# Kernel tuning notes

Measured on AMD Instinct MI355X. Metric: run time of the kernel, lower is better.

Reference implementation:

```python
import jax, jax.numpy as jnp
import numpy as np

HEADS = 16
LN_EPS = 1e-5


def setup_inputs() -> dict:
    key = jax.random.key(0)
    ks = jax.random.split(key, 12)
    B, IMG, Q, H = 8192, 2048, 768, 1024
    def init(k, shape, fan_in):
        return jax.random.normal(k, shape, dtype=jnp.float32) * (fan_in ** -0.5)
    return {
        "features1": jax.random.normal(ks[0], (B, IMG), dtype=jnp.float32),
        "features2": jax.random.normal(ks[1], (B, Q), dtype=jnp.float32),
        "W1": init(ks[2], (IMG, H), IMG),
        "b1": jnp.zeros((H,), dtype=jnp.float32),
        "W2": init(ks[3], (Q, H), Q),
        "b2": jnp.zeros((H,), dtype=jnp.float32),
        "Wqkv": init(ks[4], (H, 3 * H), H),
        "Wout": init(ks[5], (H, H), H),
        "bout": jnp.zeros((H,), dtype=jnp.float32),
        "gamma": jnp.ones((2 * H,), dtype=jnp.float32),
        "beta": jnp.zeros((2 * H,), dtype=jnp.float32),
    }


def reference(features1, features2, W1, b1, W2, b2, Wqkv, Wout, bout, gamma, beta):
    B = features1.shape[0]
    H = W1.shape[1]
    hd = H // HEADS
    scale = hd ** -0.5
    # modality projections -> [B, H] each
    f1 = features1 @ W1 + b1
    f2 = features2 @ W2 + b2
    x = jnp.stack([f1, f2], axis=1)                      # [B, 2, H]
    qkv = x @ Wqkv                                       # [B, 2, 3H]
    q, k, v = jnp.split(qkv, 3, axis=-1)
    # b n (h d) -> b h n d
    def to_heads(t):
        return t.reshape(B, 2, HEADS, hd).transpose(0, 2, 1, 3)
    q, k, v = to_heads(q) * scale, to_heads(k), to_heads(v)
    attn = jnp.einsum('bhid,bhjd->bhij', q, k)           # [B, h, 2, 2]
    attn = jax.nn.softmax(attn, axis=-1)
    out = jnp.einsum('bhij,bhjd->bhid', attn, v)         # [B, h, 2, d]
    out = out.transpose(0, 2, 1, 3).reshape(B, 2, H)     # b h n d -> b n (h d)
    out = out @ Wout + bout                              # [B, 2, H]
    flat = out.reshape(B, 2 * H)
    # LayerNorm over last dim
    mu = jnp.mean(flat, axis=-1, keepdims=True)
    var = jnp.var(flat, axis=-1, keepdims=True)
    normed = (flat - mu) * jax.lax.rsqrt(var + LN_EPS) * gamma + beta
    # dropout in eval mode = identity
    res = jnp.concatenate([f1, f2], axis=1)              # [B, 2H]
    return normed + res
```

## Files before the change

kernel.cpp:

```cpp
#include <hip/hip_runtime.h>
#include <hip/hip_bf16.h>
#include <cstdint>

typedef __attribute__((ext_vector_type(8))) short short8;
typedef __attribute__((ext_vector_type(4))) short short4v;
typedef __attribute__((ext_vector_type(4))) float floatx4;
typedef __attribute__((ext_vector_type(4))) unsigned short ushort4v;

__device__ __forceinline__ float bf2f(unsigned short u) {
    union { unsigned int u; float f; } v;
    v.u = ((unsigned int)u) << 16;
    return v.f;
}
__device__ __forceinline__ unsigned short f2bf(float f) {
    union { float f; unsigned int u; } v; v.f = f;
    unsigned int u = v.u;
    unsigned int r = (u + 0x7FFFu + ((u >> 16) & 1u)) >> 16;
    return (unsigned short)r;
}
__device__ __forceinline__ float lo_bf(unsigned int u) {
    union { unsigned int u; float f; } v; v.u = u << 16; return v.f;
}
__device__ __forceinline__ float hi_bf(unsigned int u) {
    union { unsigned int u; float f; } v; v.u = u & 0xffff0000u; return v.f;
}
__device__ __forceinline__ void gld_lds16(const void* g, void* l) {
    __builtin_amdgcn_global_load_lds(
        (const __attribute__((address_space(1))) unsigned int*)g,
        (__attribute__((address_space(3))) unsigned int*)l,
        16, 0, 0);
}

__global__ __launch_bounds__(256) void cvt_bf16_kernel(const float* __restrict__ in,
                                                       unsigned short* __restrict__ out,
                                                       int n4) {
    int i = blockIdx.x * 256 + threadIdx.x;
    if (i >= n4) return;
    float4 v = ((const float4*)in)[i];
    ushort4v o;
    o.x = f2bf(v.x); o.y = f2bf(v.y); o.z = f2bf(v.z); o.w = f2bf(v.w);
    ((ushort4v*)out)[i] = o;
}

__global__ __launch_bounds__(256) void transpose_cvt_kernel(const float* __restrict__ in,
                                                            unsigned short* __restrict__ out,
                                                            int K, int N) {
    __shared__ float tile[32][33];
    const int n0 = blockIdx.x * 32;
    const int k0 = blockIdx.y * 32;
    const int tx = threadIdx.x;
    const int ty = threadIdx.y;
#pragma unroll
    for (int i = 0; i < 32; i += 8)
        tile[ty + i][tx] = in[(size_t)(k0 + ty + i) * N + n0 + tx];
    __syncthreads();
#pragma unroll
    for (int i = 0; i < 32; i += 8)
        out[(size_t)(n0 + ty + i) * K + k0 + tx] = f2bf(tile[tx][ty + i]);
}

template <bool OUT_BF16, bool HAS_BIAS>
__global__ __launch_bounds__(256, 2)
void gemm_bt64(const unsigned short* __restrict__ A, const unsigned short* __restrict__ Bt,
               void* __restrict__ Cv, const float* __restrict__ bias,
               int M, int N, int K, int ldc) {
    __shared__ alignas(16) unsigned short As[8192];
    __shared__ alignas(16) unsigned short Bs[8192];

    const int tid  = threadIdx.x;
    const int lane = tid & 63;
    const int wave = tid >> 6;
    const int blockM = blockIdx.y * 128;
    const int blockN = blockIdx.x * 128;
    const int wm = wave >> 1, wn = wave & 1;

    const unsigned short* gA[4];
    const unsigned short* gB[4];
    unsigned short* lA[4];
    unsigned short* lB[4];
#pragma unroll
    for (int g = 0; g < 4; g++) {
        int ci = g * 256 + tid;
        int hh = ci >> 9, rem = ci & 511, row = rem >> 2, sub = rem & 3;
        gA[g] = A  + (size_t)(blockM + row) * K + hh * 32 + sub * 8;
        gB[g] = Bt + (size_t)(blockN + row) * K + hh * 32 + sub * 8;
        lA[g] = As + g * 2048 + wave * 512;
        lB[g] = Bs + g * 2048 + wave * 512;
    }

    floatx4 acc[4][4];
#pragma unroll
    for (int i = 0; i < 4; i++)
#pragma unroll
        for (int j = 0; j < 4; j++) acc[i][j] = (floatx4){0.f, 0.f, 0.f, 0.f};

    const int col  = lane & 15;
    const int quad = lane >> 4;
    const int aoff32 = (wm * 64 + col) * 32 + quad * 8;
    const int boff32 = (wn * 64 + col) * 32 + quad * 8;

    const int kIters = K >> 6;
    for (int kt = 0; kt < kIters; ++kt) {
        const size_t ko = (size_t)kt * 64;
#pragma unroll
        for (int g = 0; g < 4; g++) gld_lds16(gA[g] + ko, lA[g]);
#pragma unroll
        for (int g = 0; g < 4; g++) gld_lds16(gB[g] + ko, lB[g]);
        __syncthreads();

#pragma unroll
        for (int hh = 0; hh < 2; hh++) {
            short8 a[4], b[4];
#pragma unroll
            for (int i = 0; i < 4; i++) a[i] = *(const short8*)&As[hh * 4096 + aoff32 + i * 512];
#pragma unroll
            for (int j = 0; j < 4; j++) b[j] = *(const short8*)&Bs[hh * 4096 + boff32 + j * 512];
#pragma unroll
            for (int i = 0; i < 4; i++)
#pragma unroll
                for (int j = 0; j < 4; j++)
                    acc[i][j] = __builtin_amdgcn_mfma_f32_16x16x32_bf16(a[i], b[j], acc[i][j], 0, 0, 0);
        }
        __syncthreads();
    }

#pragma unroll
    for (int i = 0; i < 4; i++) {
#pragma unroll
        for (int j = 0; j < 4; j++) {
#pragma unroll
            for (int r = 0; r < 4; r++) {
                int row = blockM + wm * 64 + i * 16 + quad * 4 + r;
                int cn  = blockN + wn * 64 + j * 16 + col;
                float v = acc[i][j][r];
                if (HAS_BIAS) v += bias[cn];
                if (OUT_BF16) ((unsigned short*)Cv)[(size_t)row * ldc + cn] = f2bf(v);
                else          ((float*)Cv)[(size_t)row * ldc + cn] = v;
            }
        }
    }
}

#define T2_STRIDE 132
__global__ __launch_bounds__(256, 2)
void gemm_qkv_attn(const unsigned short* __restrict__ A, const unsigned short* __restrict__ Bt,
                   unsigned short* __restrict__ attn_out) {
    __shared__ alignas(16) char smem[52224];
    unsigned short* As = (unsigned short*)smem;
    unsigned short* Bs = As + 8192;
    unsigned short* T2 = (unsigned short*)smem;
    float* wsm = (float*)(smem + 50688);

    const int tid  = threadIdx.x;
    const int lane = tid & 63;
    const int wave = tid >> 6;
    const int h = blockIdx.x;
    const int blockM = blockIdx.y * 128;
    const int wm = wave >> 1, wn = wave & 1;
    const int K = 1024;

    const unsigned short* gA[4];
    unsigned short* lA[4];
#pragma unroll
    for (int g = 0; g < 4; g++) {
        int ci = g * 256 + tid;
        int hh = ci >> 9, rem = ci & 511, row = rem >> 2, sub = rem & 3;
        gA[g] = A + (size_t)(blockM + row) * K + hh * 32 + sub * 8;
        lA[g] = As + g * 2048 + wave * 512;
    }
    const unsigned short* gB[6];
    unsigned short* lB[6];
#pragma unroll
    for (int g = 0; g < 6; g++) {
        int ci = g * 256 + tid;
        int hh = (ci >= 768) ? 1 : 0;
        int rem = ci - hh * 768;
        int row = rem >> 2, sub = rem & 3;
        int sec = row >> 6, wr = row & 63;
        gB[g] = Bt + (size_t)(sec * 1024 + h * 64 + wr) * K + hh * 32 + sub * 8;
        lB[g] = Bs + g * 2048 + wave * 512;
    }

    floatx4 acc[4][6];
#pragma unroll
    for (int i = 0; i < 4; i++)
#pragma unroll
        for (int j = 0; j < 6; j++) acc[i][j] = (floatx4){0.f, 0.f, 0.f, 0.f};

    const int col  = lane & 15;
    const int quad = lane >> 4;
    const int aoff32 = (wm * 64 + col) * 32 + quad * 8;
    const int boff32 = (wn * 96 + col) * 32 + quad * 8;

    for (int kt = 0; kt < 16; ++kt) {
        const size_t ko = (size_t)kt * 64;
#pragma unroll
        for (int g = 0; g < 4; g++) gld_lds16(gA[g] + ko, lA[g]);
#pragma unroll
        for (int g = 0; g < 6; g++) gld_lds16(gB[g] + ko, lB[g]);
        __syncthreads();

#pragma unroll
        for (int hh = 0; hh < 2; hh++) {
            short8 a[4], b[6];
#pragma unroll
            for (int i = 0; i < 4; i++) a[i] = *(const short8*)&As[hh * 4096 + aoff32 + i * 512];
#pragma unroll
            for (int j = 0; j < 6; j++) b[j] = *(const short8*)&Bs[hh * 6144 + boff32 + j * 512];
#pragma unroll
            for (int i = 0; i < 4; i++)
#pragma unroll
                for (int j = 0; j < 6; j++)
                    acc[i][j] = __builtin_amdgcn_mfma_f32_16x16x32_bf16(a[i], b[j], acc[i][j], 0, 0, 0);
        }
        __syncthreads();
    }

#pragma unroll
    for (int i = 0; i < 4; i++) {
#pragma unroll
        for (int j = 0; j < 6; j++) {
            int c  = wn * 96 + j * 16 + col;
            int r0 = wm * 64 + i * 16 + quad * 4;
            short4v pk;
            pk.x = (short)f2bf(acc[i][j][0]);
            pk.y = (short)f2bf(acc[i][j][1]);
            pk.z = (short)f2bf(acc[i][j][2]);
            pk.w = (short)f2bf(acc[i][j][3]);
            *(short4v*)&T2[c * T2_STRIDE + r0] = pk;
        }
    }
    __syncthreads();

    if (tid < 64) {
        const int ib = tid;
        float s00 = 0.f, s01 = 0.f, s10 = 0.f, s11 = 0.f;
#pragma unroll 8
        for (int d = 0; d < 64; d++) {
            unsigned int qp = *(const unsigned int*)&T2[d * T2_STRIDE + 2 * ib];
            unsigned int kp = *(const unsigned int*)&T2[(64 + d) * T2_STRIDE + 2 * ib];
            float q0 = lo_bf(qp), q1 = hi_bf(qp);
            float k0 = lo_bf(kp), k1 = hi_bf(kp);
            s00 += q0 * k0; s01 += q0 * k1;
            s10 += q1 * k0; s11 += q1 * k1;
        }
        const float sc = 0.125f;
        s00 *= sc; s01 *= sc; s10 *= sc; s11 *= sc;
        float m0 = fmaxf(s00, s01), m1 = fmaxf(s10, s11);
        float e00 = __expf(s00 - m0), e01 = __expf(s01 - m0);
        float e10 = __expf(s10 - m1), e11 = __expf(s11 - m1);
        float i0 = 1.f / (e00 + e01), i1 = 1.f / (e10 + e11);
        wsm[ib * 4 + 0] = e00 * i0; wsm[ib * 4 + 1] = e01 * i0;
        wsm[ib * 4 + 2] = e10 * i1; wsm[ib * 4 + 3] = e11 * i1;
    }
    __syncthreads();

#pragma unroll
    for (int g = 0; g < 4; g++) {
        int chunk = g * 256 + tid;
        int r = chunk >> 3;
        int dc = (chunk & 7) * 8;
        int ib = r >> 1, n = r & 1;
        float w0 = wsm[ib * 4 + n * 2 + 0];
        float w1 = wsm[ib * 4 + n * 2 + 1];
        short8 o;
#pragma unroll
        for (int dd = 0; dd < 8; dd++) {
            unsigned int vp = *(const unsigned int*)&T2[(128 + dc + dd) * T2_STRIDE + 2 * ib];
            o[dd] = (short)f2bf(w0 * lo_bf(vp) + w1 * hi_bf(vp));
        }
        *(short8*)&attn_out[(size_t)(blockM + r) * 1024 + h * 64 + dc] = o;
    }
}

__global__ __launch_bounds__(256) void ln_res_kernel(const unsigned short* __restrict__ proj,
                                                     const unsigned short* __restrict__ xres,
                                                     const float* __restrict__ gamma,
                                                     const float* __restrict__ beta,
                                                     float* __restrict__ out) {
    const int b = blockIdx.x;
    const int tid = threadIdx.x;
    const size_t base = (size_t)b * 2048;
    short8 p8 = ((const short8*)(proj + base))[tid];
    float pv[8];
#pragma unroll
    for (int e = 0; e < 8; e++) pv[e] = bf2f((unsigned short)p8[e]);
    float s = 0.f, ss = 0.f;
#pragma unroll
    for (int e = 0; e < 8; e++) { s += pv[e]; ss += pv[e] * pv[e]; }
#pragma unroll
    for (int off = 32; off > 0; off >>= 1) {
        s  += __shfl_xor(s, off);
        ss += __shfl_xor(ss, off);
    }
    __shared__ float red[8];
    const int wave = tid >> 6;
    if ((tid & 63) == 0) { red[wave] = s; red[4 + wave] = ss; }
    __syncthreads();
    s  = red[0] + red[1] + red[2] + red[3];
    ss = red[4] + red[5] + red[6] + red[7];
    const float mean = s * (1.0f / 2048.0f);
    const float var  = ss * (1.0f / 2048.0f) - mean * mean;
    const float rstd = rsqrtf(var + 1e-5f);

    const float4* g4 = (const float4*)gamma;
    const float4* b4 = (const float4*)beta;
    float4 g0 = g4[2 * tid], g1 = g4[2 * tid + 1];
    float4 be0 = b4[2 * tid], be1 = b4[2 * tid + 1];
    short8 r8 = ((const short8*)(xres + base))[tid];
    float4 o0, o1;
    o0.x = (pv[0] - mean) * rstd * g0.x + be0.x + bf2f((unsigned short)r8[0]);
    o0.y = (pv[1] - mean) * rstd * g0.y + be0.y + bf2f((unsigned short)r8[1]);
    o0.z = (pv[2] - mean) * rstd * g0.z + be0.z + bf2f((unsigned short)r8[2]);
    o0.w = (pv[3] - mean) * rstd * g0.w + be0.w + bf2f((unsigned short)r8[3]);
    o1.x = (pv[4] - mean) * rstd * g1.x + be1.x + bf2f((unsigned short)r8[4]);
    o1.y = (pv[5] - mean) * rstd * g1.y + be1.y + bf2f((unsigned short)r8[5]);
    o1.z = (pv[6] - mean) * rstd * g1.z + be1.z + bf2f((unsigned short)r8[6]);
    o1.w = (pv[7] - mean) * rstd * g1.w + be1.w + bf2f((unsigned short)r8[7]);
    float4* op = (float4*)(out + base);
    op[2 * tid] = o0;
    op[2 * tid + 1] = o1;
}

extern "C" void kernel_launch(void* const* d_in, const int* in_sizes, int n_in,
                              void* d_out, int out_size, void* d_ws, size_t ws_size,
                              hipStream_t stream) {
    (void)in_sizes; (void)n_in; (void)out_size; (void)ws_size;
    const float* features1 = (const float*)d_in[0];
    const float* features2 = (const float*)d_in[1];
    const float* W1   = (const float*)d_in[2];
    const float* b1   = (const float*)d_in[3];
    const float* W2   = (const float*)d_in[4];
    const float* b2   = (const float*)d_in[5];
    const float* Wqkv = (const float*)d_in[6];
    const float* Wout = (const float*)d_in[7];
    const float* bout = (const float*)d_in[8];
    const float* gamma = (const float*)d_in[9];
    const float* beta  = (const float*)d_in[10];
    float* out = (float*)d_out;

    char* ws = (char*)d_ws;
    unsigned short* f1b   = (unsigned short*)(ws);
    unsigned short* f2b   = (unsigned short*)(ws + 33554432);
    unsigned short* W1t   = (unsigned short*)(ws + 46137344);
    unsigned short* W2t   = (unsigned short*)(ws + 50331648);
    unsigned short* Wqkvt = (unsigned short*)(ws + 51904512);
    unsigned short* Woutt = (unsigned short*)(ws + 58195968);
    unsigned short* xb    = (unsigned short*)(ws + 60293120);
    unsigned short* attn  = (unsigned short*)(ws + 93847552);
    unsigned short* projb = (unsigned short*)(ws + 127401984);

    cvt_bf16_kernel<<<16384, 256, 0, stream>>>(features1, f1b, 8192 * 2048 / 4);
    cvt_bf16_kernel<<<6144, 256, 0, stream>>>(features2, f2b, 8192 * 768 / 4);

    transpose_cvt_kernel<<<dim3(1024 / 32, 2048 / 32), dim3(32, 8), 0, stream>>>(W1, W1t, 2048, 1024);
    transpose_cvt_kernel<<<dim3(1024 / 32, 768 / 32),  dim3(32, 8), 0, stream>>>(W2, W2t, 768, 1024);
    transpose_cvt_kernel<<<dim3(3072 / 32, 1024 / 32), dim3(32, 8), 0, stream>>>(Wqkv, Wqkvt, 1024, 3072);
    transpose_cvt_kernel<<<dim3(1024 / 32, 1024 / 32), dim3(32, 8), 0, stream>>>(Wout, Woutt, 1024, 1024);

    gemm_bt64<true, true><<<dim3(8, 64), 256, 0, stream>>>(
        f1b, W1t, (void*)xb, b1, 8192, 1024, 2048, 2048);
    gemm_bt64<true, true><<<dim3(8, 64), 256, 0, stream>>>(
        f2b, W2t, (void*)(xb + 1024), b2, 8192, 1024, 768, 2048);
    gemm_qkv_attn<<<dim3(16, 128), 256, 0, stream>>>(xb, Wqkvt, attn);
    gemm_bt64<true, true><<<dim3(8, 128), 256, 0, stream>>>(
        attn, Woutt, (void*)projb, bout, 16384, 1024, 1024, 1024);
    ln_res_kernel<<<8192, 256, 0, stream>>>(projb, xb, gamma, beta, out);
}
```

Baseline: 405.1 us.

## Merge conversion/transpose launches and fuse two projection GEMMs into one grid

Six conversion and transpose kernels are merged into a single prep kernel that dispatches on block index. The two modality projection GEMMs are combined into one launch using blockIdx.z. Global-to-LDS address setup is simplified to one base pointer plus fixed strides, and launch bounds request higher occupancy. The goal is to cut launch overhead and tail gaps between small kernels, at the risk of register pressure from the raised occupancy targets.

Result: no change. 398.6 us (-1.6%).

```diff
diff --git a/kernel.cpp b/kernel.cpp
--- a/kernel.cpp
+++ b/kernel.cpp
@@ -31,42 +31,56 @@
         16, 0, 0);
 }
 
-__global__ __launch_bounds__(256) void cvt_bf16_kernel(const float* __restrict__ in,
-                                                       unsigned short* __restrict__ out,
-                                                       int n4) {
-    int i = blockIdx.x * 256 + threadIdx.x;
-    if (i >= n4) return;
-    float4 v = ((const float4*)in)[i];
-    ushort4v o;
-    o.x = f2bf(v.x); o.y = f2bf(v.y); o.z = f2bf(v.z); o.w = f2bf(v.w);
-    ((ushort4v*)out)[i] = o;
-}
-
-__global__ __launch_bounds__(256) void transpose_cvt_kernel(const float* __restrict__ in,
-                                                            unsigned short* __restrict__ out,
-                                                            int K, int N) {
+__global__ __launch_bounds__(256) void prep_kernel(
+    const float* __restrict__ f1, const float* __restrict__ f2,
+    unsigned short* __restrict__ f1b, unsigned short* __restrict__ f2b,
+    const float* __restrict__ W1, unsigned short* __restrict__ W1t,
+    const float* __restrict__ W2, unsigned short* __restrict__ W2t,
+    const float* __restrict__ Wqkv, unsigned short* __restrict__ Wqkvt,
+    const float* __restrict__ Wout, unsigned short* __restrict__ Woutt) {
     __shared__ float tile[32][33];
-    const int n0 = blockIdx.x * 32;
-    const int k0 = blockIdx.y * 32;
-    const int tx = threadIdx.x;
-    const int ty = threadIdx.y;
+    const int b = blockIdx.x;
+    const int tid = threadIdx.x;
+
+    if (b < 5632) {
+        const float* in = (b < 4096) ? f1 : f2;
+        unsigned short* outp = (b < 4096) ? f1b : f2b;
+        int base = ((b < 4096) ? b : (b - 4096)) * 1024 + tid;
+#pragma unroll
+        for (int it = 0; it < 4; it++) {
+            int i = base + it * 256;
+            float4 v = ((const float4*)in)[i];
+            ushort4v o;
+            o.x = f2bf(v.x); o.y = f2bf(v.y); o.z = f2bf(v.z); o.w = f2bf(v.w);
+            ((ushort4v*)outp)[i] = o;
+        }
+        return;
+    }
+
+    const float* in; unsigned short* outp; int K, N, t;
+    if (b < 7680)       { in = W1;   outp = W1t;   K = 2048; N = 1024; t = b - 5632;  }
+    else if (b < 8448)  { in = W2;   outp = W2t;   K = 768;  N = 1024; t = b - 7680;  }
+    else if (b < 11520) { in = Wqkv; outp = Wqkvt; K = 1024; N = 3072; t = b - 8448;  }
+    else                { in = Wout; outp = Woutt; K = 1024; N = 1024; t = b - 11520; }
+    const int ntiles = N >> 5;
+    const int n0 = (t % ntiles) * 32;
+    const int k0 = (t / ntiles) * 32;
+    const int tx = tid & 31, ty = tid >> 5;
 #pragma unroll
     for (int i = 0; i < 32; i += 8)
         tile[ty + i][tx] = in[(size_t)(k0 + ty + i) * N + n0 + tx];
     __syncthreads();
 #pragma unroll
     for (int i = 0; i < 32; i += 8)
-        out[(size_t)(n0 + ty + i) * K + k0 + tx] = f2bf(tile[tx][ty + i]);
+        outp[(size_t)(n0 + ty + i) * K + k0 + tx] = f2bf(tile[tx][ty + i]);
 }
 
 template <bool OUT_BF16, bool HAS_BIAS>
-__global__ __launch_bounds__(256, 2)
-void gemm_bt64(const unsigned short* __restrict__ A, const unsigned short* __restrict__ Bt,
-               void* __restrict__ Cv, const float* __restrict__ bias,
-               int M, int N, int K, int ldc) {
-    __shared__ alignas(16) unsigned short As[8192];
-    __shared__ alignas(16) unsigned short Bs[8192];
-
+__device__ __forceinline__ void gemm_core(const unsigned short* __restrict__ A,
+                                          const unsigned short* __restrict__ Bt,
+                                          void* __restrict__ Cv, const float* __restrict__ bias,
+                                          int K, int ldc,
+                                          unsigned short* As, unsigned short* Bs) {
     const int tid  = threadIdx.x;
     const int lane = tid & 63;
     const int wave = tid >> 6;
@@ -74,19 +88,11 @@
     const int blockN = blockIdx.x * 128;
     const int wm = wave >> 1, wn = wave & 1;
 
-    const unsigned short* gA[4];
-    const unsigned short* gB[4];
-    unsigned short* lA[4];
-    unsigned short* lB[4];
-#pragma unroll
-    for (int g = 0; g < 4; g++) {
-        int ci = g * 256 + tid;
-        int hh = ci >> 9, rem = ci & 511, row = rem >> 2, sub = rem & 3;
-        gA[g] = A  + (size_t)(blockM + row) * K + hh * 32 + sub * 8;
-        gB[g] = Bt + (size_t)(blockN + row) * K + hh * 32 + sub * 8;
-        lA[g] = As + g * 2048 + wave * 512;
-        lB[g] = Bs + g * 2048 + wave * 512;
-    }
+    const unsigned short* gA = A  + (size_t)(blockM + (tid >> 2)) * K + (tid & 3) * 8;
+    const unsigned short* gB = Bt + (size_t)(blockN + (tid >> 2)) * K + (tid & 3) * 8;
+    const size_t sK = (size_t)64 * K;
+    unsigned short* lA = As + wave * 512;
+    unsigned short* lB = Bs + wave * 512;
 
     floatx4 acc[4][4];
 #pragma unroll
@@ -102,24 +108,28 @@
     const int kIters = K >> 6;
     for (int kt = 0; kt < kIters; ++kt) {
         const size_t ko = (size_t)kt * 64;
-#pragma unroll
-        for (int g = 0; g < 4; g++) gld_lds16(gA[g] + ko, lA[g]);
-#pragma unroll
-        for (int g = 0; g < 4; g++) gld_lds16(gB[g] + ko, lB[g]);
+        gld_lds16(gA + ko,           lA);
+        gld_lds16(gA + sK + ko,      lA + 2048);
+        gld_lds16(gA + 32 + ko,      lA + 4096);
+        gld_lds16(gA + sK + 32 + ko, lA + 6144);
+        gld_lds16(gB + ko,           lB);
+        gld_lds16(gB + sK + ko,      lB + 2048);
+        gld_lds16(gB + 32 + ko,      lB + 4096);
+        gld_lds16(gB + sK + 32 + ko, lB + 6144);
         __syncthreads();
 
 #pragma unroll
         for (int hh = 0; hh < 2; hh++) {
-            short8 a[4], b[4];
+            short8 a[4], bf[4];
 #pragma unroll
             for (int i = 0; i < 4; i++) a[i] = *(const short8*)&As[hh * 4096 + aoff32 + i * 512];
 #pragma unroll
-            for (int j = 0; j < 4; j++) b[j] = *(const short8*)&Bs[hh * 4096 + boff32 + j * 512];
+            for (int j = 0; j < 4; j++) bf[j] = *(const short8*)&Bs[hh * 4096 + boff32 + j * 512];
 #pragma unroll
             for (int i = 0; i < 4; i++)
 #pragma unroll
                 for (int j = 0; j < 4; j++)
-                    acc[i][j] = __builtin_amdgcn_mfma_f32_16x16x32_bf16(a[i], b[j], acc[i][j], 0, 0, 0);
+                    acc[i][j] = __builtin_amdgcn_mfma_f32_16x16x32_bf16(a[i], bf[j], acc[i][j], 0, 0, 0);
         }
         __syncthreads();
     }
@@ -141,8 +151,29 @@
     }
 }
 
+__global__ __launch_bounds__(256, 4)
+void gemm_f12(const unsigned short* __restrict__ f1b, const unsigned short* __restrict__ W1t,
+              const float* __restrict__ b1,
+              const unsigned short* __restrict__ f2b, const unsigned short* __restrict__ W2t,
+              const float* __restrict__ b2, unsigned short* __restrict__ xb) {
+    __shared__ alignas(16) unsigned short As[8192];
+    __shared__ alignas(16) unsigned short Bs[8192];
+    if (blockIdx.z == 0)
+        gemm_core<true, true>(f1b, W1t, (void*)xb, b1, 2048, 2048, As, Bs);
+    else
+        gemm_core<true, true>(f2b, W2t, (void*)(xb + 1024), b2, 768, 2048, As, Bs);
+}
+
+__global__ __launch_bounds__(256, 4)
+void gemm_proj(const unsigned short* __restrict__ attn, const unsigned short* __restrict__ Woutt,
+               const float* __restrict__ bout, unsigned short* __restrict__ projb) {
+    __shared__ alignas(16) unsigned short As[8192];
+    __shared__ alignas(16) unsigned short Bs[8192];
+    gemm_core<true, true>(attn, Woutt, (void*)projb, bout, 1024, 1024, As, Bs);
+}
+
 #define T2_STRIDE 132
-__global__ __launch_bounds__(256, 2)
+__global__ __launch_bounds__(256, 3)
 void gemm_qkv_attn(const unsigned short* __restrict__ A, const unsigned short* __restrict__ Bt,
                    unsigned short* __restrict__ attn_out) {
     __shared__ alignas(16) char smem[52224];
@@ -159,27 +190,10 @@
     const int wm = wave >> 1, wn = wave & 1;
     const int K = 1024;
 
-    const unsigned short* gA[4];
-    unsigned short* lA[4];
-#pragma unroll
-    for (int g = 0; g < 4; g++) {
-        int ci = g * 256 + tid;
-        int hh = ci >> 9, rem = ci & 511, row = rem >> 2, sub = rem & 3;
-        gA[g] = A + (size_t)(blockM + row) * K + hh * 32 + sub * 8;
-        lA[g] = As + g * 2048 + wave * 512;
-    }
-    const unsigned short* gB[6];
-    unsigned short* lB[6];
-#pragma unroll
-    for (int g = 0; g < 6; g++) {
-        int ci = g * 256 + tid;
-        int hh = (ci >= 768) ? 1 : 0;
-        int rem = ci - hh * 768;
-        int row = rem >> 2, sub = rem & 3;
-        int sec = row >> 6, wr = row & 63;
-        gB[g] = Bt + (size_t)(sec * 1024 + h * 64 + wr) * K + hh * 32 + sub * 8;
-        lB[g] = Bs + g * 2048 + wave * 512;
-    }
+    const unsigned short* gA = A  + (size_t)(blockM + (tid >> 2)) * K + (tid & 3) * 8;
+    const unsigned short* gB = Bt + (size_t)(h * 64 + (tid >> 2)) * K + (tid & 3) * 8;
+    unsigned short* lA = As + wave * 512;
+    unsigned short* lB = Bs + wave * 512;
 
     floatx4 acc[4][6];
 #pragma unroll
@@ -194,24 +208,30 @@
 
     for (int kt = 0; kt < 16; ++kt) {
         const size_t ko = (size_t)kt * 64;
-#pragma unroll
-        for (int g = 0; g < 4; g++) gld_lds16(gA[g] + ko, lA[g]);
-#pragma unroll
-        for (int g = 0; g < 6; g++) gld_lds16(gB[g] + ko, lB[g]);
+        gld_lds16(gA + ko,               lA);
+        gld_lds16(gA + 65536 + ko,       lA + 2048);
+        gld_lds16(gA + 32 + ko,          lA + 4096);
+        gld_lds16(gA + 65536 + 32 + ko,  lA + 6144);
+        gld_lds16(gB + ko,               lB);
+        gld_lds16(gB + 1048576 + ko,     lB + 2048);
+        gld_lds16(gB + 2097152 + ko,     lB + 4096);
+        gld_lds16(gB + 32 + ko,          lB + 6144);
+        gld_lds16(gB + 1048576 + 32 + ko, lB + 8192);
+        gld_lds16(gB + 2097152 + 32 + ko, lB + 10240);
         __syncthreads();
 
 #pragma unroll
         for (int hh = 0; hh < 2; hh++) {
-            short8 a[4], b[6];
+            short8 a[4], bf[6];
 #pragma unroll
             for (int i = 0; i < 4; i++) a[i] = *(const short8*)&As[hh * 4096 + aoff32 + i * 512];
 #pragma unroll
-            for (int j = 0; j < 6; j++) b[j] = *(const short8*)&Bs[hh * 6144 + boff32 + j * 512];
+            for (int j = 0; j < 6; j++) bf[j] = *(const short8*)&Bs[hh * 6144 + boff32 + j * 512];
 #pragma unroll
             for (int i = 0; i < 4; i++)
 #pragma unroll
                 for (int j = 0; j < 6; j++)
-                    acc[i][j] = __builtin_amdgcn_mfma_f32_16x16x32_bf16(a[i], b[j], acc[i][j], 0, 0, 0);
+                    acc[i][j] = __builtin_amdgcn_mfma_f32_16x16x32_bf16(a[i], bf[j], acc[i][j], 0, 0, 0);
         }
         __syncthreads();
     }
@@ -350,20 +370,10 @@
     unsigned short* attn  = (unsigned short*)(ws + 93847552);
     unsigned short* projb = (unsigned short*)(ws + 127401984);
 
-    cvt_bf16_kernel<<<16384, 256, 0, stream>>>(features1, f1b, 8192 * 2048 / 4);
-    cvt_bf16_kernel<<<6144, 256, 0, stream>>>(features2, f2b, 8192 * 768 / 4);
-
-    transpose_cvt_kernel<<<dim3(1024 / 32, 2048 / 32), dim3(32, 8), 0, stream>>>(W1, W1t, 2048, 1024);
-    transpose_cvt_kernel<<<dim3(1024 / 32, 768 / 32),  dim3(32, 8), 0, stream>>>(W2, W2t, 768, 1024);
-    transpose_cvt_kernel<<<dim3(3072 / 32, 1024 / 32), dim3(32, 8), 0, stream>>>(Wqkv, Wqkvt, 1024, 3072);
-    transpose_cvt_kernel<<<dim3(1024 / 32, 1024 / 32), dim3(32, 8), 0, stream>>>(Wout, Woutt, 1024, 1024);
-
-    gemm_bt64<true, true><<<dim3(8, 64), 256, 0, stream>>>(
-        f1b, W1t, (void*)xb, b1, 8192, 1024, 2048, 2048);
-    gemm_bt64<true, true><<<dim3(8, 64), 256, 0, stream>>>(
-        f2b, W2t, (void*)(xb + 1024), b2, 8192, 1024, 768, 2048);
+    prep_kernel<<<12544, 256, 0, stream>>>(features1, features2, f1b, f2b,
+                                           W1, W1t, W2, W2t, Wqkv, Wqkvt, Wout, Woutt);
+    gemm_f12<<<dim3(8, 64, 2), 256, 0, stream>>>(f1b, W1t, b1, f2b, W2t, b2, xb);
     gemm_qkv_attn<<<dim3(16, 128), 256, 0, stream>>>(xb, Wqkvt, attn);
-    gemm_bt64<true, true><<<dim3(8, 128), 256, 0, stream>>>(
-        attn, Woutt, (void*)projb, bout, 16384, 1024, 1024, 1024);
+    gemm_proj<<<dim3(8, 128), 256, 0, stream>>>(attn, Woutt, bout, projb);
     ln_res_kernel<<<8192, 256, 0, stream>>>(projb, xb, gamma, beta, out);
 }
```
